# Kernel tuning notes

Measured on AMD Instinct MI355X. Metric: run time of the kernel, lower is better.

## Reference

```python
import jax, jax.numpy as jnp
import numpy as np

RADIUS = 0.4
MAX_SAMPLES = 32  # max_samples_per_octant


def setup_inputs() -> dict:
    key = jax.random.key(0)
    pcs = jax.random.normal(key, (4, 3, 2048), dtype=jnp.float32)
    return {"pcs": pcs}


def octant_query(pcs, radius, K):
    """pcs: [B, 3, N] -> indices [B, N, 9, K] int64.

    For each center point i, neighbors j (j != i) with ||p_j - p_i|| < radius are
    binned into one of 8 octants by the sign of (p_j - p_i); the first K such j
    (in ascending index order, matching a sequential CUDA scan) fill each octant's
    slots, remaining slots padded with the center index i. Octant 9 (index 8)
    holds the center index i itself.
    """
    B, _, N = pcs.shape
    p = jnp.transpose(pcs, (0, 2, 1))  # [B, N, 3]
    # Per-coordinate pairwise differences: d*[b, i, j] = p_j - p_i
    dx = p[:, None, :, 0] - p[:, :, None, 0]  # [B, N, N]
    dy = p[:, None, :, 1] - p[:, :, None, 1]
    dz = p[:, None, :, 2] - p[:, :, None, 2]
    dist2 = dx * dx + dy * dy + dz * dz
    not_self = ~jnp.eye(N, dtype=bool)[None]
    within = (dist2 < radius * radius) & not_self  # [B, N, N]
    oct_code = ((dx > 0).astype(jnp.int32)
                + 2 * (dy > 0).astype(jnp.int32)
                + 4 * (dz > 0).astype(jnp.int32))  # [B, N, N] in 0..7

    center = jnp.arange(N, dtype=jnp.int64)
    # out has K+1 slots per octant; slot K is a dump for overflow/invalid writes.
    out = jnp.broadcast_to(center[None, :, None, None], (B, N, 9, K + 1))

    b_idx = jnp.arange(B)[:, None, None]
    i_idx = jnp.arange(N)[None, :, None]
    j_vals = jnp.broadcast_to(jnp.arange(N, dtype=jnp.int64)[None, None, :], (B, N, N))

    for o in range(8):  # fixed small structural loop over octants
        m = within & (oct_code == o)            # [B, N, N]
        rank = jnp.cumsum(m.astype(jnp.int32), axis=-1) - 1  # order of arrival
        slot = jnp.where(m & (rank < K), rank, K)             # invalid -> dump slot
        out = out.at[b_idx, i_idx, o, slot].set(j_vals)
    return out[..., :K]  # drop dump slot -> [B, N, 9, K]


def reference(pcs):
    return octant_query(pcs, RADIUS, MAX_SAMPLES)
```

## Files before the change

kernel.cpp:

```cpp
#include <hip/hip_runtime.h>
#include <cstdint>


#define NPTS   2048
#define KSAMP  32
#define RAD2   0.16f

__device__ __forceinline__ unsigned rank_below(unsigned long long mask) {
    return __builtin_amdgcn_mbcnt_hi((unsigned)(mask >> 32),
           __builtin_amdgcn_mbcnt_lo((unsigned)(mask & 0xffffffffu), 0u));
}

__global__ __launch_bounds__(256) void octant_query_kernel(
    const float* __restrict__ pcs, int* __restrict__ out, int nwaves) {
#pragma clang fp contract(off)
    const int wave = (int)((blockIdx.x * blockDim.x + threadIdx.x) >> 6);
    const int lane = (int)(threadIdx.x & 63);
    if (wave >= nwaves) return;
    const int b = wave >> 11;
    const int i = wave & (NPTS - 1);

    const float* __restrict__ px = pcs + (size_t)b * 3 * NPTS;
    const float* __restrict__ py = px + NPTS;
    const float* __restrict__ pz = py + NPTS;

    const float cx = px[i];
    const float cy = py[i];
    const float cz = pz[i];

    int* __restrict__ obase = out + (size_t)(b * NPTS + i) * 9 * KSAMP;

    int cnt0 = 0, cnt1 = 0, cnt2 = 0, cnt3 = 0;
    int cnt4 = 0, cnt5 = 0, cnt6 = 0, cnt7 = 0;

    for (int c = 0; c < NPTS; c += 64) {
        const int j = c + lane;
        const float dx = px[j] - cx;
        const float dy = py[j] - cy;
        const float dz = pz[j] - cz;
        float d2 = dx * dx;
        d2 = d2 + dy * dy;
        d2 = d2 + dz * dz;
        const bool within = (d2 < RAD2) && (j != i);
        const unsigned long long mw = __ballot(within);
        if (mw == 0ULL) continue;

        const unsigned long long mx = __ballot(dx > 0.f);
        const unsigned long long my = __ballot(dy > 0.f);
        const unsigned long long mz = __ballot(dz > 0.f);

#define DO_OCT(o, cnt)                                                      \
        {                                                                   \
            unsigned long long m = mw;                                      \
            m &= ((o) & 1) ? mx : ~mx;                                      \
            m &= ((o) & 2) ? my : ~my;                                      \
            m &= ((o) & 4) ? mz : ~mz;                                      \
            if (m) {                                      \
                const bool mine = (m >> lane) & 1ULL;                       \
                if (mine) {                                                 \
                    const int r = cnt + (int)rank_below(m);                 \
                    if (r < KSAMP) obase[(o) * KSAMP + r] = j;              \
                }                                                           \
                cnt += (int)__popcll(m);                                    \
            }                                                               \
        }
        DO_OCT(0, cnt0) DO_OCT(1, cnt1) DO_OCT(2, cnt2) DO_OCT(3, cnt3)
        DO_OCT(4, cnt4) DO_OCT(5, cnt5) DO_OCT(6, cnt6) DO_OCT(7, cnt7)
#undef DO_OCT
    }

#define FILL(o, cnt)                                                        \
        {                                                                   \
            const int s = cnt + lane;                                       \
            if (s < KSAMP) obase[(o) * KSAMP + s] = i;                      \
        }
    FILL(0, cnt0) FILL(1, cnt1) FILL(2, cnt2) FILL(3, cnt3)
    FILL(4, cnt4) FILL(5, cnt5) FILL(6, cnt6) FILL(7, cnt7)
#undef FILL
    if (lane < KSAMP) obase[8 * KSAMP + lane] = i;
}

extern "C" void kernel_launch(void* const* d_in, const int* in_sizes, int n_in,
                              void* d_out, int out_size, void* d_ws, size_t ws_size,
                              hipStream_t stream) {
    const float* pcs = (const float*)d_in[0];
    int* out = (int*)d_out;
    const int B = in_sizes[0] / (3 * NPTS);
    const int nwaves = B * NPTS;
    const int block = 256;
    const int grid = (nwaves * 64 + block - 1) / block;
    octant_query_kernel<<<grid, block, 0, stream>>>(pcs, out, nwaves);
}
```

Before: 70.20 us.

## Stage batch point cloud in LDS and prefetch next chunk per wave

Each block of 8 waves now copies the whole batch's 2048 points into shared memory with float4 loads, and each wave reads neighbour candidates from LDS instead of global memory. The next chunk's coordinates are loaded one iteration early to hide latency. The self-exclusion test becomes a ballot mask applied only on the center's chunk. The cost is 24KB of LDS per block plus a full reload of the batch per block, which may limit occupancy, and the float4 staging assumes exactly 512 threads per block covering NPTS.

```diff
diff --git a/kernel.cpp b/kernel.cpp
--- a/kernel.cpp
+++ b/kernel.cpp
@@ -5,49 +5,81 @@
 #define NPTS   2048
 #define KSAMP  32
 #define RAD2   0.16f
+#define WPB    8
+#define BLOCK  (WPB * 64)
 
 __device__ __forceinline__ unsigned rank_below(unsigned long long mask) {
     return __builtin_amdgcn_mbcnt_hi((unsigned)(mask >> 32),
            __builtin_amdgcn_mbcnt_lo((unsigned)(mask & 0xffffffffu), 0u));
 }
 
-__global__ __launch_bounds__(256) void octant_query_kernel(
+__global__ __launch_bounds__(BLOCK) void octant_query_kernel(
     const float* __restrict__ pcs, int* __restrict__ out, int nwaves) {
 #pragma clang fp contract(off)
-    const int wave = (int)((blockIdx.x * blockDim.x + threadIdx.x) >> 6);
-    const int lane = (int)(threadIdx.x & 63);
-    if (wave >= nwaves) return;
-    const int b = wave >> 11;
-    const int i = wave & (NPTS - 1);
+    __shared__ float sx[NPTS];
+    __shared__ float sy[NPTS];
+    __shared__ float sz[NPTS];
+
+    const int tid  = (int)threadIdx.x;
+    const int wid  = tid >> 6;
+    const int lane = tid & 63;
+    const int wave = (int)blockIdx.x * WPB + wid;
+    const int b    = (wave - wid) >> 11;
 
     const float* __restrict__ px = pcs + (size_t)b * 3 * NPTS;
     const float* __restrict__ py = px + NPTS;
     const float* __restrict__ pz = py + NPTS;
 
-    const float cx = px[i];
-    const float cy = py[i];
-    const float cz = pz[i];
+    {
+        const float4 vx = ((const float4*)px)[tid];
+        const float4 vy = ((const float4*)py)[tid];
+        const float4 vz = ((const float4*)pz)[tid];
+        ((float4*)sx)[tid] = vx;
+        ((float4*)sy)[tid] = vy;
+        ((float4*)sz)[tid] = vz;
+    }
+    __syncthreads();
+
+    if (wave >= nwaves) return;
+
+    const int i = wave & (NPTS - 1);
+    const float cx = sx[i];
+    const float cy = sy[i];
+    const float cz = sz[i];
 
     int* __restrict__ obase = out + (size_t)(b * NPTS + i) * 9 * KSAMP;
+    const int ichunk = i >> 6;
+    const unsigned long long notself = ~(1ULL << (i & 63));
 
     int cnt0 = 0, cnt1 = 0, cnt2 = 0, cnt3 = 0;
     int cnt4 = 0, cnt5 = 0, cnt6 = 0, cnt7 = 0;
 
+    float jx = sx[lane];
+    float jy = sy[lane];
+    float jz = sz[lane];
+
     for (int c = 0; c < NPTS; c += 64) {
-        const int j = c + lane;
-        const float dx = px[j] - cx;
-        const float dy = py[j] - cy;
-        const float dz = pz[j] - cz;
+        const float dx = jx - cx;
+        const float dy = jy - cy;
+        const float dz = jz - cz;
+
+        const int cn = (c + 64) & (NPTS - 1);
+        jx = sx[cn + lane];
+        jy = sy[cn + lane];
+        jz = sz[cn + lane];
+
         float d2 = dx * dx;
         d2 = d2 + dy * dy;
         d2 = d2 + dz * dz;
-        const bool within = (d2 < RAD2) && (j != i);
-        const unsigned long long mw = __ballot(within);
+
+        unsigned long long mw = __ballot(d2 < RAD2);
+        if ((c >> 6) == ichunk) mw &= notself;
         if (mw == 0ULL) continue;
 
         const unsigned long long mx = __ballot(dx > 0.f);
         const unsigned long long my = __ballot(dy > 0.f);
         const unsigned long long mz = __ballot(dz > 0.f);
+        const int j = c + lane;
 
 #define DO_OCT(o, cnt)                                                      \
         {                                                                   \
@@ -87,7 +119,6 @@
     int* out = (int*)d_out;
     const int B = in_sizes[0] / (3 * NPTS);
     const int nwaves = B * NPTS;
-    const int block = 256;
-    const int grid = (nwaves * 64 + block - 1) / block;
-    octant_query_kernel<<<grid, block, 0, stream>>>(pcs, out, nwaves);
+    const int grid = nwaves / WPB;
+    octant_query_kernel<<<grid, BLOCK, 0, stream>>>(pcs, out, nwaves);
 }
```

New measurement: 77.33 us. 10.2% more time.

## Process two center points per wave and remap blocks across batches

Applied to the files above, without the earlier changes.

Each wave now handles two adjacent center points, so each candidate point is loaded once and reused for both distance tests. Only the within-radius ballot is taken up front; the self-exclusion mask is applied just on the center's own chunk, and the sign ballots are taken only when a center has hits. When the grid is 1024 blocks, block indices are remapped so neighbouring blocks cover different batches. The catch is half as many waves, more registers for two sets of counters, and a layout that assumes B*N is divisible by 8.

```diff
diff --git a/kernel.cpp b/kernel.cpp
--- a/kernel.cpp
+++ b/kernel.cpp
@@ -12,72 +12,131 @@
 }
 
 __global__ __launch_bounds__(256) void octant_query_kernel(
-    const float* __restrict__ pcs, int* __restrict__ out, int nwaves) {
+    const float* __restrict__ pcs, int* __restrict__ out) {
 #pragma clang fp contract(off)
-    const int wave = (int)((blockIdx.x * blockDim.x + threadIdx.x) >> 6);
+    const int wid  = (int)(threadIdx.x >> 6);
     const int lane = (int)(threadIdx.x & 63);
-    if (wave >= nwaves) return;
-    const int b = wave >> 11;
-    const int i = wave & (NPTS - 1);
+    const int m    = (int)blockIdx.x;
+
+    int b, pair;
+    if (gridDim.x == 1024) {
+        const int low = m & 255;
+        b    = low >> 6;
+        pair = (((m >> 8) << 6) | (low & 63)) * 4 + wid;
+    } else {
+        const int w = m * 4 + wid;
+        b    = w >> 10;
+        pair = w & 1023;
+    }
+    const int i0 = pair * 2;
+    const int i1 = i0 + 1;
 
     const float* __restrict__ px = pcs + (size_t)b * 3 * NPTS;
     const float* __restrict__ py = px + NPTS;
     const float* __restrict__ pz = py + NPTS;
 
-    const float cx = px[i];
-    const float cy = py[i];
-    const float cz = pz[i];
+    const float cx0 = px[i0], cy0 = py[i0], cz0 = pz[i0];
+    const float cx1 = px[i1], cy1 = py[i1], cz1 = pz[i1];
 
-    int* __restrict__ obase = out + (size_t)(b * NPTS + i) * 9 * KSAMP;
+    int* __restrict__ obase0 = out + (size_t)(b * NPTS + i0) * 9 * KSAMP;
+    int* __restrict__ obase1 = out + (size_t)(b * NPTS + i1) * 9 * KSAMP;
 
-    int cnt0 = 0, cnt1 = 0, cnt2 = 0, cnt3 = 0;
-    int cnt4 = 0, cnt5 = 0, cnt6 = 0, cnt7 = 0;
+    const int ichunk0 = i0 >> 6;
+    const int ichunk1 = i1 >> 6;
+    const unsigned long long notself0 = ~(1ULL << (i0 & 63));
+    const unsigned long long notself1 = ~(1ULL << (i1 & 63));
+
+    int cA0 = 0, cA1 = 0, cA2 = 0, cA3 = 0, cA4 = 0, cA5 = 0, cA6 = 0, cA7 = 0;
+    int cB0 = 0, cB1 = 0, cB2 = 0, cB3 = 0, cB4 = 0, cB5 = 0, cB6 = 0, cB7 = 0;
+
+#define DO_OCT(ob, o, mexpr, cnt)                                           \
+        {                                                                   \
+            const unsigned long long mm = (mexpr);                          \
+            if (mm) {                                     \
+                if ((mm >> lane) & 1ULL) {                                  \
+                    const int r = cnt + (int)rank_below(mm);                \
+                    if (r < KSAMP) (ob)[(o) * KSAMP + r] = j;               \
+                }                                                           \
+                cnt += (int)__popcll(mm);                                   \
+            }                                                               \
+        }
+
+#define OCTS(ob, mw, mx, my, mz, c0, c1, c2, c3, c4, c5, c6, c7)            \
+        {                                                                   \
+            const unsigned long long a0 = (mw) & ~(mx), a1 = (mw) & (mx);   \
+            const unsigned long long b0 = a0 & ~(my), b1 = a1 & ~(my);      \
+            const unsigned long long b2 = a0 &  (my), b3 = a1 &  (my);      \
+            DO_OCT(ob, 0, b0 & ~(mz), c0)                                   \
+            DO_OCT(ob, 1, b1 & ~(mz), c1)                                   \
+            DO_OCT(ob, 2, b2 & ~(mz), c2)                                   \
+            DO_OCT(ob, 3, b3 & ~(mz), c3)                                   \
+            DO_OCT(ob, 4, b0 &  (mz), c4)                                   \
+            DO_OCT(ob, 5, b1 &  (mz), c5)                                   \
+            DO_OCT(ob, 6, b2 &  (mz), c6)                                   \
+            DO_OCT(ob, 7, b3 &  (mz), c7)                                   \
+        }
 
     for (int c = 0; c < NPTS; c += 64) {
+        const float xx = px[c + lane];
+        const float yy = py[c + lane];
+        const float zz = pz[c + lane];
+
+        const float dx0 = xx - cx0;
+        const float dy0 = yy - cy0;
+        const float dz0 = zz - cz0;
+        float d20 = dx0 * dx0;
+        d20 = d20 + dy0 * dy0;
+        d20 = d20 + dz0 * dz0;
+
+        const float dx1 = xx - cx1;
+        const float dy1 = yy - cy1;
+        const float dz1 = zz - cz1;
+        float d21 = dx1 * dx1;
+        d21 = d21 + dy1 * dy1;
+        d21 = d21 + dz1 * dz1;
+
+        unsigned long long mw0 = __ballot(d20 < RAD2);
+        unsigned long long mw1 = __ballot(d21 < RAD2);
+        const int ch = c >> 6;
+        if (ch == ichunk0) mw0 &= notself0;
+        if (ch == ichunk1) mw1 &= notself1;
+        if ((mw0 | mw1) == 0ULL) continue;
+
         const int j = c + lane;
-        const float dx = px[j] - cx;
-        const float dy = py[j] - cy;
-        const float dz = pz[j] - cz;
-        float d2 = dx * dx;
-        d2 = d2 + dy * dy;
-        d2 = d2 + dz * dz;
-        const bool within = (d2 < RAD2) && (j != i);
-        const unsigned long long mw = __ballot(within);
-        if (mw == 0ULL) continue;
+        if (mw0) {
+            const unsigned long long mx = __ballot(dx0 > 0.f);
+            const unsigned long long my = __ballot(dy0 > 0.f);
+            const unsigned long long mz = __ballot(dz0 > 0.f);
+            OCTS(obase0, mw0, mx, my, mz, cA0, cA1, cA2, cA3, cA4, cA5, cA6, cA7)
+        }
+        if (mw1) {
+            const unsigned long long mx = __ballot(dx1 > 0.f);
+            const unsigned long long my = __ballot(dy1 > 0.f);
+            const unsigned long long mz = __ballot(dz1 > 0.f);
+            OCTS(obase1, mw1, mx, my, mz, cB0, cB1, cB2, cB3, cB4, cB5, cB6, cB7)
+        }
+    }
+#undef OCTS
+#undef DO_OCT
 
-        const unsigned long long mx = __ballot(dx > 0.f);
-        const unsigned long long my = __ballot(dy > 0.f);
-        const unsigned long long mz = __ballot(dz > 0.f);
-
-#define DO_OCT(o, cnt)                                                      \
-        {                                                                   \
-            unsigned long long m = mw;                                      \
-            m &= ((o) & 1) ? mx : ~mx;                                      \
-            m &= ((o) & 2) ? my : ~my;                                      \
-            m &= ((o) & 4) ? mz : ~mz;                                      \
-            if (m) {                                      \
-                const bool mine = (m >> lane) & 1ULL;                       \
-                if (mine) {                                                 \
-                    const int r = cnt + (int)rank_below(m);                 \
-                    if (r < KSAMP) obase[(o) * KSAMP + r] = j;              \
-                }                                                           \
-                cnt += (int)__popcll(m);                                    \
-            }                                                               \
-        }
-        DO_OCT(0, cnt0) DO_OCT(1, cnt1) DO_OCT(2, cnt2) DO_OCT(3, cnt3)
-        DO_OCT(4, cnt4) DO_OCT(5, cnt5) DO_OCT(6, cnt6) DO_OCT(7, cnt7)
-#undef DO_OCT
-    }
-
-#define FILL(o, cnt)                                                        \
+#define FILL(ob, idx, o, cnt)                                               \
         {                                                                   \
             const int s = cnt + lane;                                       \
-            if (s < KSAMP) obase[(o) * KSAMP + s] = i;                      \
+            if (s < KSAMP) (ob)[(o) * KSAMP + s] = idx;                     \
         }
-    FILL(0, cnt0) FILL(1, cnt1) FILL(2, cnt2) FILL(3, cnt3)
-    FILL(4, cnt4) FILL(5, cnt5) FILL(6, cnt6) FILL(7, cnt7)
+    FILL(obase0, i0, 0, cA0) FILL(obase0, i0, 1, cA1)
+    FILL(obase0, i0, 2, cA2) FILL(obase0, i0, 3, cA3)
+    FILL(obase0, i0, 4, cA4) FILL(obase0, i0, 5, cA5)
+    FILL(obase0, i0, 6, cA6) FILL(obase0, i0, 7, cA7)
+    FILL(obase1, i1, 0, cB0) FILL(obase1, i1, 1, cB1)
+    FILL(obase1, i1, 2, cB2) FILL(obase1, i1, 3, cB3)
+    FILL(obase1, i1, 4, cB4) FILL(obase1, i1, 5, cB5)
+    FILL(obase1, i1, 6, cB6) FILL(obase1, i1, 7, cB7)
 #undef FILL
-    if (lane < KSAMP) obase[8 * KSAMP + lane] = i;
+    if (lane < KSAMP) {
+        obase0[8 * KSAMP + lane] = i0;
+        obase1[8 * KSAMP + lane] = i1;
+    }
 }
 
 extern "C" void kernel_launch(void* const* d_in, const int* in_sizes, int n_in,
@@ -86,8 +145,8 @@
     const float* pcs = (const float*)d_in[0];
     int* out = (int*)d_out;
     const int B = in_sizes[0] / (3 * NPTS);
-    const int nwaves = B * NPTS;
+    const int npairs = B * NPTS / 2;
     const int block = 256;
-    const int grid = (nwaves * 64 + block - 1) / block;
-    octant_query_kernel<<<grid, block, 0, stream>>>(pcs, out, nwaves);
+    const int grid = npairs / 4;
+    octant_query_kernel<<<grid, block, 0, stream>>>(pcs, out);
 }
```

Result: slower. 85.08 us (+21.2%).
